# Kernel tuning notes

Measured on AMD Instinct MI355X. Metric: run time of the kernel, lower is better.

The kernel has to match this reference:

```python
import jax, jax.numpy as jnp
import numpy as np

B, S, D, H, MB = 2, 2048, 2048, 32, 16
HD = D // H          # 64
N = S // MB          # 128 mini-batches
EPS = 1e-5
BASE_LR = 1.0


def setup_inputs() -> dict:
    ks = jax.random.split(jax.random.key(0), 8)
    sc = 1.0 / np.sqrt(D)
    inv = 1.0 / (10000.0 ** (np.arange(0, HD, 2, dtype=np.float64) / HD))
    return {
        "x": jax.random.normal(ks[0], (B, S, D), jnp.float32),
        "pos_frequencies": jnp.asarray(np.outer(np.arange(S), inv), jnp.float32),  # (S, HD//2) rope angles
        "Wq": jax.random.normal(ks[1], (D, D), jnp.float32) * sc,
        "Wk": jax.random.normal(ks[2], (D, D), jnp.float32) * sc,
        "Wv": jax.random.normal(ks[3], (D, D), jnp.float32) * sc,
        "Wo": jax.random.normal(ks[4], (D, D), jnp.float32) * sc,
        "post_gamma": jnp.ones((D,), jnp.float32),
        "post_beta": jnp.zeros((D,), jnp.float32),
        "ilr_W": jax.random.normal(ks[5], (H, 1, D), jnp.float32) * 0.02,  # inner_loop_lr_W
        "ilr_b": jnp.zeros((H, 1), jnp.float32),                            # inner_loop_lr_b
        "lgs": jnp.zeros((MB,), jnp.float32),                               # learnable_gradient_scale
        "ttt_gamma": jnp.ones((H, HD), jnp.float32),                        # ttt_norm_weight
        "ttt_beta": jnp.zeros((H, HD), jnp.float32),                        # ttt_norm_bias
        "W0": jax.random.normal(ks[6], (H, HD, HD), jnp.float32) / np.sqrt(HD),
        "b0": jnp.zeros((H, 1, HD), jnp.float32),
    }


def _rope(x, freqs):
    # x: (B,H,S,HD), freqs: (S,HD//2); rotate interleaved pairs
    cos = jnp.cos(freqs)[None, None]
    sin = jnp.sin(freqs)[None, None]
    x1, x2 = x[..., 0::2], x[..., 1::2]
    return jnp.stack([x1 * cos - x2 * sin, x1 * sin + x2 * cos], -1).reshape(x.shape)


def _ln_fwd(z, g, b):
    mu = z.mean(-1, keepdims=True)
    var = z.var(-1, keepdims=True)
    return g * (z - mu) * jax.lax.rsqrt(var + EPS) + b


def _ln_l2_bwd(z, tgt, g, b):
    # grad of 0.5*||LN(z) - tgt||^2 w.r.t. z (fused LayerNorm backward)
    mu = z.mean(-1, keepdims=True)
    var = z.var(-1, keepdims=True)
    rstd = jax.lax.rsqrt(var + EPS)
    zh = (z - mu) * rstd
    dy = (g * zh + b) - tgt
    dzh = dy * g
    return (dzh - dzh.mean(-1, keepdims=True) - zh * (dzh * zh).mean(-1, keepdims=True)) * rstd


def reference(x, pos_frequencies, Wq, Wk, Wv, Wo, post_gamma, post_beta,
              ilr_W, ilr_b, lgs, ttt_gamma, ttt_beta, W0, b0):
    # projections (torch Linear: x @ W.T), shape (B,H,S,HD)
    q = (x @ Wq.T).reshape(B, S, H, HD).transpose(0, 2, 1, 3)
    k = (x @ Wk.T).reshape(B, S, H, HD).transpose(0, 2, 1, 3)
    v = (x @ Wv.T).reshape(B, S, H, HD).transpose(0, 2, 1, 3)
    q = _rope(q, pos_frequencies)
    k = _rope(k, pos_frequencies)
    v = _rope(v, pos_frequencies)  # module applies RoPE to V too

    # inner-loop learning rates: (B,H,N,1,MB), gradient_scale: (MB,1)
    xr = x.reshape(B, N, MB, D)
    lr = jnp.einsum('bnkd,hod->bhnko', xr, ilr_W) + ilr_b.reshape(1, H, 1, 1, 1)
    lr = BASE_LR * jax.nn.sigmoid(lr).transpose(0, 1, 2, 4, 3) / HD
    gs = jnp.clip(1.0 / jnp.arange(1, MB + 1, dtype=jnp.float32) + lgs, 0.0)
    eta = gs.reshape(1, 1, 1, MB, 1) * lr  # (B,H,N,MB,MB)

    to_n = lambda t: t.reshape(B, H, N, MB, -1).transpose(2, 0, 1, 3, 4)
    Qn, Kn, Vn = to_n(q), to_n(k), to_n(v)           # (N,B,H,MB,HD)
    En = eta.transpose(2, 0, 1, 3, 4)                # (N,B,H,MB,MB)

    g = ttt_gamma.reshape(1, H, 1, HD)
    be = ttt_beta.reshape(1, H, 1, HD)
    W_init = jnp.broadcast_to(W0[None], (B, H, HD, HD))
    b_init = jnp.broadcast_to(b0[None], (B, H, 1, HD))

    def step(carry, inp):
        W, bb = carry
        XQ, XK, XV, E = inp
        Z = XK @ W + bb
        grad = _ln_l2_bwd(Z, XV - XK, g, be)                 # (B,H,MB,HD)
        Attn = jnp.tril(XQ @ XK.swapaxes(-1, -2))            # causal dual form
        b_bar = bb - jnp.tril(E) @ grad
        Z_bar = XQ @ W - (E * Attn) @ grad + b_bar
        last_eta = E[..., -1, :, None]                       # (B,H,MB,1)
        W_new = W - jnp.swapaxes(last_eta * XK, -1, -2) @ grad
        b_new = bb - jnp.sum(last_eta * grad, axis=-2, keepdims=True)
        return (W_new, b_new), XQ + _ln_fwd(Z_bar, g, be)

    _, ys = jax.lax.scan(step, (W_init, b_init), (Qn, Kn, Vn, En))  # ys: (N,B,H,MB,HD)
    out = ys.transpose(1, 0, 3, 2, 4).reshape(B, S, D)

    mu = out.mean(-1, keepdims=True)
    var = out.var(-1, keepdims=True)
    out = post_gamma * (out - mu) * jax.lax.rsqrt(var + EPS) + post_beta
    return out @ Wo.T
```

## Files before the change

kernel.cpp:

```cpp
#include <hip/hip_runtime.h>
#include <hip/hip_bf16.h>
#include <math.h>

#define BB 2
#define SS 2048
#define DD 2048
#define HH 32
#define HDD 64
#define MBB 16
#define NN 128

typedef unsigned short u16;
typedef short bf16x8_t __attribute__((ext_vector_type(8)));
typedef float f32x4_t __attribute__((ext_vector_type(4)));

__device__ __forceinline__ float b2f(u16 u) { return __uint_as_float(((unsigned)u) << 16); }
__device__ __forceinline__ u16 f2b(float f) {
    unsigned u = __float_as_uint(f);
    return (u16)((u + 0x7FFFu + ((u >> 16) & 1u)) >> 16);
}
__device__ __forceinline__ unsigned pk2(float a, float b) {
    return (unsigned)f2b(a) | ((unsigned)f2b(b) << 16);
}
__device__ __forceinline__ unsigned cvtpk(float lo, float hi) {
    unsigned r;
    asm("v_cvt_pk_bf16_f32 %0, %1, %2" : "=v"(r) : "v"(lo), "v"(hi));
    return r;
}
__device__ __forceinline__ unsigned pk2r(u16 a, u16 b) { return (unsigned)a | ((unsigned)b << 16); }
__device__ __forceinline__ float wsum(float x) {
    x += __shfl_xor(x, 32);
    x += __shfl_xor(x, 16);
    x += __shfl_xor(x, 8);
    x += __shfl_xor(x, 4);
    x += __shfl_xor(x, 2);
    x += __shfl_xor(x, 1);
    return x;
}

template <int CTRL>
__device__ __forceinline__ float dppadd(float x) {
    int t = __builtin_amdgcn_update_dpp(0, __float_as_int(x), CTRL, 0xF, 0xF, true);
    return x + __int_as_float(t);
}
__device__ __forceinline__ float rsum16(float x) {
    x = dppadd<0xB1>(x);
    x = dppadd<0x4E>(x);
    x = dppadd<0x141>(x);
    x = dppadd<0x140>(x);
    return x;
}

typedef __attribute__((address_space(3))) unsigned int lds_u32;
typedef __attribute__((address_space(1))) const unsigned int glb_u32;
__device__ __forceinline__ void async_copy16(const void* g, void* l) {
    __builtin_amdgcn_global_load_lds((glb_u32*)g, (lds_u32*)l, 16, 0, 0);
}


__global__ __launch_bounds__(256) void k_cvt5(const float* __restrict__ x, const float* __restrict__ wq,
                                              const float* __restrict__ wk, const float* __restrict__ wv,
                                              const float* __restrict__ wo, u16* __restrict__ xb,
                                              u16* __restrict__ wqb, u16* __restrict__ wkb,
                                              u16* __restrict__ wvb, u16* __restrict__ wob) {
    int sl = blockIdx.y;
    long e = (long)(blockIdx.x * 256 + threadIdx.x) * 4;
    if (sl == 5) {
        long n = e >> 11;
        int cin = (int)(e & 2047);
        int hd0 = (cin >> 6) * 64 + ((cin & 63) >> 2);
        const float* src = wo + n * 2048 + hd0;
        float f0 = src[0], f1 = src[16], f2 = src[32], f3 = src[48];
        uint2 o;
        o.x = pk2(f0, f1);
        o.y = pk2(f2, f3);
        *(uint2*)(wob + e) = o;
        return;
    }
    const float* s;
    u16* d;
    if (sl == 0) { s = x; d = xb; }
    else if (sl == 1) { s = x + 4194304; d = xb + 4194304; }
    else if (sl == 2) { s = wq; d = wqb; }
    else if (sl == 3) { s = wk; d = wkb; }
    else { s = wv; d = wvb; }
    float4 f = *(const float4*)(s + e);
    uint2 o;
    o.x = pk2(f.x, f.y);
    o.y = pk2(f.z, f.w);
    *(uint2*)(d + e) = o;
}

__global__ void k_trig(const float* __restrict__ pf, float* __restrict__ ct, float* __restrict__ st) {
    int i = blockIdx.x * 256 + threadIdx.x;
    float f = pf[i];
    ct[i] = cosf(f);
    st[i] = sinf(f);
}

__global__ void k_ppg(const float* __restrict__ pg, const float* __restrict__ pb,
                      float* __restrict__ pgp, float* __restrict__ pbp) {
    int i = blockIdx.x * 256 + threadIdx.x;
    int h = i >> 6, o = i & 63;
    int src = h * 64 + (o >> 2) + (o & 3) * 16;
    pgp[i] = pg[src];
    pbp[i] = pb[src];
}

template <int EPI>
__global__ __launch_bounds__(256) void k_gemm_bt(const u16* __restrict__ A, const u16* __restrict__ B0,
                                                 const u16* __restrict__ B1, const u16* __restrict__ B2,
                                                 void* __restrict__ C0, void* __restrict__ C1,
                                                 void* __restrict__ C2, int M, int Nn, int K,
                                                 const float* __restrict__ ct, const float* __restrict__ st) {
    __shared__ u16 As[128 * 32];
    __shared__ u16 Bs[128 * 32];
    int z = blockIdx.z;
    const u16* Bm = (z == 0) ? B0 : (z == 1) ? B1 : B2;
    void* Cout = (z == 0) ? C0 : (z == 1) ? C1 : C2;
    int tid = threadIdx.x, lane = tid & 63, wv = tid >> 6;
    int m0 = blockIdx.y * 128, n0 = blockIdx.x * 128;
    int wm = wv >> 1, wn = wv & 1;

    f32x4_t acc[4][4];
    f32x4_t zero = {0.f, 0.f, 0.f, 0.f};
#pragma unroll
    for (int a = 0; a < 4; ++a)
#pragma unroll
        for (int b = 0; b < 4; ++b) acc[a][b] = zero;

    int mrow = lane & 15, qk = (lane >> 4) * 8;
    const int kTiles = K >> 5;
    for (int kt = 0; kt < kTiles; ++kt) {
        __syncthreads();
        int kb = kt << 5;
#pragma unroll
        for (int it = 0; it < 2; ++it) {
            int cb = it * 256 + wv * 64;
            int c = cb + lane;
            const u16* gpA = A + (m0 + (c >> 2)) * K + kb + ((c & 3) << 3);
            async_copy16(gpA, &As[cb << 3]);
            const u16* gpB = Bm + (n0 + (c >> 2)) * K + kb + ((c & 3) << 3);
            async_copy16(gpB, &Bs[cb << 3]);
        }
        asm volatile("s_waitcnt vmcnt(0)" ::: "memory");
        __syncthreads();

        bf16x8_t af[4], bfr[4];
#pragma unroll
        for (int mi = 0; mi < 4; ++mi)
            af[mi] = *(const bf16x8_t*)&As[(wm * 64 + mi * 16 + mrow) * 32 + qk];
#pragma unroll
        for (int ni = 0; ni < 4; ++ni)
            bfr[ni] = *(const bf16x8_t*)&Bs[(wn * 64 + ni * 16 + mrow) * 32 + qk];
#pragma unroll
        for (int mi = 0; mi < 4; ++mi)
#pragma unroll
            for (int ni = 0; ni < 4; ++ni)
                acc[mi][ni] = __builtin_amdgcn_mfma_f32_16x16x32_bf16(af[mi], bfr[ni], acc[mi][ni], 0, 0, 0);
    }

    int col16 = lane & 15, rq = (lane >> 4) * 4;
#pragma unroll
    for (int mi = 0; mi < 4; ++mi) {
#pragma unroll
        for (int ni = 0; ni < 4; ++ni) {
#pragma unroll
            for (int r = 0; r < 4; ++r) {
                int gr = m0 + wm * 64 + mi * 16 + rq + r;
                int gc = n0 + wn * 64 + ni * 16 + col16;
                float val = acc[mi][ni][r];
                if (EPI == 0) {
                    ((float*)Cout)[gr * Nn + gc] = val;
                } else {
                    int b = gr >> 11, s2 = gr & 2047, hh = gc >> 6, hd = gc & 63;
                    int fi = s2 * 32 + (hd >> 1);
                    float c = ct[fi], sn = st[fi];
                    float partner = __shfl_xor(val, 1);
                    float y = (gc & 1) ? (partner * sn + val * c) : (val * c - partner * sn);
                    int po = (z == 2) ? ((hd & 15) * 4 + (hd >> 4)) : hd;
                    ((u16*)Cout)[(((b * HH + hh) * SS) + s2) * HDD + po] = f2b(y);
                }
            }
        }
    }
}

__global__ __launch_bounds__(256) void k_lr(const u16* __restrict__ xb, const float* __restrict__ ilrW,
                                            const float* __restrict__ ilrb, float* __restrict__ lrout) {
    __shared__ u16 xr[4][2048];
    int row0 = blockIdx.x * 4;
    int tid = threadIdx.x, lane = tid & 63, wv = tid >> 6;
    const unsigned* src = (const unsigned*)(xb + row0 * 2048);
    unsigned* dst = (unsigned*)xr;
    for (int i = tid; i < 4096; i += 256) dst[i] = src[i];
    __syncthreads();
    int b = row0 >> 11, s0 = row0 & 2047;
#pragma unroll
    for (int sub = 0; sub < 8; ++sub) {
        int h = wv * 8 + sub;
        const float* wp = ilrW + h * 2048;
        float a0 = 0.f, a1 = 0.f, a2 = 0.f, a3 = 0.f;
        for (int i = 0; i < 16; ++i) {
            int idx = i * 128 + lane * 2;
            float2 w2 = *(const float2*)(wp + idx);
            unsigned p0 = *(const unsigned*)&xr[0][idx];
            unsigned p1 = *(const unsigned*)&xr[1][idx];
            unsigned p2 = *(const unsigned*)&xr[2][idx];
            unsigned p3 = *(const unsigned*)&xr[3][idx];
            a0 += b2f((u16)p0) * w2.x + b2f((u16)(p0 >> 16)) * w2.y;
            a1 += b2f((u16)p1) * w2.x + b2f((u16)(p1 >> 16)) * w2.y;
            a2 += b2f((u16)p2) * w2.x + b2f((u16)(p2 >> 16)) * w2.y;
            a3 += b2f((u16)p3) * w2.x + b2f((u16)(p3 >> 16)) * w2.y;
        }
        a0 = wsum(a0);
        a1 = wsum(a1);
        a2 = wsum(a2);
        a3 = wsum(a3);
        if (lane == 0) {
            float bv = ilrb[h];
            float* op = lrout + ((b * HH + h) * SS) + s0;
            op[0] = (1.0f / (1.0f + expf(-(a0 + bv)))) * (1.0f / 64.0f);
            op[1] = (1.0f / (1.0f + expf(-(a1 + bv)))) * (1.0f / 64.0f);
            op[2] = (1.0f / (1.0f + expf(-(a2 + bv)))) * (1.0f / 64.0f);
            op[3] = (1.0f / (1.0f + expf(-(a3 + bv)))) * (1.0f / 64.0f);
        }
    }
}

__global__ __launch_bounds__(64, 1) void k_scan(const u16* __restrict__ qb, const u16* __restrict__ kb2,
                                                const u16* __restrict__ vc, const float* __restrict__ lrbuf,
                                                const float* __restrict__ lgs, const float* __restrict__ tg,
                                                const float* __restrict__ tb, const float* __restrict__ W0,
                                                const float* __restrict__ b0, u16* __restrict__ ys) {
    __shared__ u16 WbL[64 * 72];
    __shared__ u16 XKT[64 * 40];
    __shared__ u16 GST[64 * 40];
    __shared__ u16 PUL[16 * 40];

    const int bh = blockIdx.x, h = bh & 31, b = bh >> 5;
    const int lane = threadIdx.x & 63;
    const int quad = lane >> 4, col = lane & 15;
    const int base = bh * SS;

    {
        unsigned* p1 = (unsigned*)XKT;
        unsigned* p2 = (unsigned*)GST;
        unsigned* p3 = (unsigned*)PUL;
        for (int i = lane; i < 1280; i += 64) { p1[i] = 0; p2[i] = 0; }
        for (int i = lane; i < 320; i += 64) p3[i] = 0;
    }

    float gd4[4], bd4[4], bbv[4], g2[4], gb[4];
#pragma unroll
    for (int tn = 0; tn < 4; ++tn) {
        gd4[tn] = tg[h * 64 + tn * 16 + col];
        bd4[tn] = tb[h * 64 + tn * 16 + col];
        bbv[tn] = b0[h * 64 + tn * 16 + col];
        g2[tn] = gd4[tn] * gd4[tn];
        gb[tn] = gd4[tn] * bd4[tn];
    }
    float G2m;
    {
        float s = g2[0] + g2[1] + g2[2] + g2[3];
        s = rsum16(s);
        G2m = s * (1.f / 64.f);
    }
    float gs4[4];
#pragma unroll
    for (int r = 0; r < 4; ++r) {
        int i = quad * 4 + r;
        gs4[r] = fmaxf(1.f / (float)(i + 1) + lgs[i], 0.f);
    }
    const float gs15 = fmaxf(1.f / 16.f + lgs[15], 0.f);

    f32x4_t Wc[4][4];
#pragma unroll
    for (int tm = 0; tm < 4; ++tm)
#pragma unroll
        for (int tn = 0; tn < 4; ++tn)
#pragma unroll
            for (int r = 0; r < 4; ++r)
                Wc[tm][tn][r] = W0[h * 4096 + (tm * 16 + quad * 4 + r) * 64 + tn * 16 + col];

    {
        unsigned* wb32 = (unsigned*)WbL;
#pragma unroll
        for (int tn = 0; tn < 4; ++tn)
#pragma unroll
            for (int tm = 0; tm < 4; ++tm) {
                int a = (tn * 16 + col) * 36 + tm * 8 + quad * 2;
                wb32[a] = cvtpk(Wc[tm][tn][0], Wc[tm][tn][1]);
                wb32[a + 1] = cvtpk(Wc[tm][tn][2], Wc[tm][tn][3]);
            }
    }

    bf16x8_t ka[2], qa[2];
    float lr4[4];
    u16 kraw[16], vraw[16], qraw[16];
    {
        const u16* kp = kb2 + (base + col) * 64;
        const u16* qp = qb + (base + col) * 64;
#pragma unroll
        for (int kh = 0; kh < 2; ++kh) {
            ka[kh] = *(const bf16x8_t*)(kp + kh * 32 + quad * 8);
            qa[kh] = *(const bf16x8_t*)(qp + kh * 32 + quad * 8);
        }
#pragma unroll
        for (int r = 0; r < 4; ++r) lr4[r] = lrbuf[base + quad * 4 + r];
#pragma unroll
        for (int tn = 0; tn < 4; ++tn)
#pragma unroll
            for (int r = 0; r < 4; ++r) {
                int idx = (base + quad * 4 + r) * 64 + tn * 16 + col;
                kraw[tn * 4 + r] = kb2[idx];
                qraw[tn * 4 + r] = qb[idx];
            }
#pragma unroll
        for (int r = 0; r < 4; ++r) {
            long ro = (long)(base + quad * 4 + r) * 64 + col * 4;
            ushort4 tv = *(const ushort4*)(vc + ro);
            vraw[r] = tv.x; vraw[4 + r] = tv.y; vraw[8 + r] = tv.z; vraw[12 + r] = tv.w;
        }
    }

    bf16x8_t xkf[4], wbf[4][2];
    {
        unsigned* x32 = (unsigned*)XKT;
#pragma unroll
        for (int tn = 0; tn < 4; ++tn) {
            int a = (tn * 16 + col) * 20 + quad * 2;
            x32[a] = pk2r(kraw[tn * 4 + 0], kraw[tn * 4 + 1]);
            x32[a + 1] = pk2r(kraw[tn * 4 + 2], kraw[tn * 4 + 3]);
        }
#pragma unroll
        for (int t = 0; t < 4; ++t)
            xkf[t] = *(const bf16x8_t*)&XKT[(t * 16 + col) * 40 + quad * 8];
#pragma unroll
        for (int tn = 0; tn < 4; ++tn)
#pragma unroll
            for (int kh = 0; kh < 2; ++kh)
                wbf[tn][kh] = *(const bf16x8_t*)&WbL[(tn * 16 + col) * 72 + kh * 32 + quad * 8];
    }

    const f32x4_t zf = {0.f, 0.f, 0.f, 0.f};

    for (int n = 0; n < NN; ++n) {
        const int s0 = n * 16;

        f32x4_t z[4], xqw[4], attn;
#pragma unroll
        for (int tn = 0; tn < 4; ++tn) {
            z[tn] = __builtin_amdgcn_mfma_f32_16x16x32_bf16(ka[1], wbf[tn][1], zf, 0, 0, 0);
            z[tn] = __builtin_amdgcn_mfma_f32_16x16x32_bf16(ka[0], wbf[tn][0], z[tn], 0, 0, 0);
            xqw[tn] = __builtin_amdgcn_mfma_f32_16x16x32_bf16(qa[1], wbf[tn][1], zf, 0, 0, 0);
            xqw[tn] = __builtin_amdgcn_mfma_f32_16x16x32_bf16(qa[0], wbf[tn][0], xqw[tn], 0, 0, 0);
        }
        attn = __builtin_amdgcn_mfma_f32_16x16x32_bf16(qa[1], ka[1], zf, 0, 0, 0);
        attn = __builtin_amdgcn_mfma_f32_16x16x32_bf16(qa[0], ka[0], attn, 0, 0, 0);

#pragma unroll
        for (int r = 0; r < 4; ++r) {
            float pv = (col <= quad * 4 + r) ? (1.f + attn[r]) : 0.f;
            PUL[(quad * 4 + r) * 40 + col] = f2b(pv);
        }

        bf16x8_t nka[2], nqa[2];
        float nlr[4];
        u16 nkraw[16], nvraw[16], nqraw[16];
        {
            const int sp = (n + 1 < NN) ? s0 + 16 : s0;
            const u16* kp = kb2 + (base + sp + col) * 64;
            const u16* qp = qb + (base + sp + col) * 64;
#pragma unroll
            for (int kh = 0; kh < 2; ++kh) {
                nka[kh] = *(const bf16x8_t*)(kp + kh * 32 + quad * 8);
                nqa[kh] = *(const bf16x8_t*)(qp + kh * 32 + quad * 8);
            }
#pragma unroll
            for (int r = 0; r < 4; ++r) nlr[r] = lrbuf[base + sp + quad * 4 + r];
#pragma unroll
            for (int tn = 0; tn < 4; ++tn)
#pragma unroll
                for (int r = 0; r < 4; ++r) {
                    int idx = (base + sp + quad * 4 + r) * 64 + tn * 16 + col;
                    nkraw[tn * 4 + r] = kb2[idx];
                    nqraw[tn * 4 + r] = qb[idx];
                }
#pragma unroll
            for (int r = 0; r < 4; ++r) {
                long ro = (long)(base + sp + quad * 4 + r) * 64 + col * 4;
                ushort4 tv = *(const ushort4*)(vc + ro);
                nvraw[r] = tv.x; nvraw[4 + r] = tv.y; nvraw[8 + r] = tv.z; nvraw[12 + r] = tv.w;
            }
        }

#pragma unroll
        for (int tn = 0; tn < 4; ++tn)
#pragma unroll
            for (int r = 0; r < 4; ++r) z[tn][r] += bbv[tn];

        float c1[16];
        float A1[4], A2[4], A3[4], A4[4], A5[4], A6[4];
#pragma unroll
        for (int r = 0; r < 4; ++r) { A1[r] = 0.f; A2[r] = 0.f; A3[r] = 0.f; A4[r] = 0.f; A5[r] = 0.f; A6[r] = 0.f; }
#pragma unroll
        for (int tn = 0; tn < 4; ++tn)
#pragma unroll
            for (int r = 0; r < 4; ++r) {
                float zv = z[tn][r];
                float tgt = b2f(vraw[tn * 4 + r]) - b2f(kraw[tn * 4 + r]);
                float c = gb[tn] - gd4[tn] * tgt;
                c1[tn * 4 + r] = c;
                float t = g2[tn] * zv;
                A1[r] += zv;
                A2[r] = fmaf(zv, zv, A2[r]);
                A3[r] += t;
                A4[r] = fmaf(t, zv, A4[r]);
                A5[r] = fmaf(c, zv, A5[r]);
                A6[r] += c;
            }
#pragma unroll
        for (int r = 0; r < 4; ++r) {
            A1[r] = rsum16(A1[r]);
            A2[r] = rsum16(A2[r]);
            A3[r] = rsum16(A3[r]);
            A4[r] = rsum16(A4[r]);
            A5[r] = rsum16(A5[r]);
            A6[r] = rsum16(A6[r]);
        }
        float mu4[4], rstd4[4], m1[4], m2[4], rl[4];
#pragma unroll
        for (int r = 0; r < 4; ++r) {
            float mu = A1[r] * (1.f / 64.f);
            float var = A2[r] * (1.f / 64.f) - mu * mu;
            float rstd = rsqrtf(var + 1e-5f);
            float T1m = A3[r] * (1.f / 64.f);
            float T2m = A4[r] * (1.f / 64.f);
            float T3m = A5[r] * (1.f / 64.f);
            float C1m = A6[r] * (1.f / 64.f);
            m1[r] = rstd * (T1m - mu * G2m) + C1m;
            m2[r] = rstd * rstd * (T2m - 2.f * mu * T1m + mu * mu * G2m) + rstd * (T3m - mu * C1m);
            mu4[r] = mu;
            rstd4[r] = rstd;
            rl[r] = rstd * lr4[r];
        }
        float gS[4][4];
#pragma unroll
        for (int tn = 0; tn < 4; ++tn)
#pragma unroll
            for (int r = 0; r < 4; ++r) {
                float zh = (z[tn][r] - mu4[r]) * rstd4[r];
                float dzh = fmaf(g2[tn], zh, c1[tn * 4 + r]);
                gS[tn][r] = fmaf(-m2[r], zh, dzh - m1[r]) * rl[r];
            }
        {
            unsigned* g32 = (unsigned*)GST;
#pragma unroll
            for (int tn = 0; tn < 4; ++tn) {
                int a = (tn * 16 + col) * 20 + quad * 2;
                g32[a] = cvtpk(gS[tn][0], gS[tn][1]);
                g32[a + 1] = cvtpk(gS[tn][2], gS[tn][3]);
            }
        }

        bf16x8_t gsf[4], puf;
#pragma unroll
        for (int t = 0; t < 4; ++t)
            gsf[t] = *(const bf16x8_t*)&GST[(t * 16 + col) * 40 + quad * 8];
        puf = *(const bf16x8_t*)&PUL[col * 40 + quad * 8];

#pragma unroll
        for (int tm = 0; tm < 4; ++tm)
#pragma unroll
            for (int tn = 0; tn < 4; ++tn) {
                f32x4_t dw = __builtin_amdgcn_mfma_f32_16x16x32_bf16(xkf[tm], gsf[tn], zf, 0, 0, 0);
#pragma unroll
                for (int r = 0; r < 4; ++r) Wc[tm][tn][r] -= gs15 * dw[r];
            }
        {
            unsigned* wb32 = (unsigned*)WbL;
#pragma unroll
            for (int tn = 0; tn < 4; ++tn)
#pragma unroll
                for (int tm = 0; tm < 4; ++tm) {
                    int a = (tn * 16 + col) * 36 + tm * 8 + quad * 2;
                    wb32[a] = cvtpk(Wc[tm][tn][0], Wc[tm][tn][1]);
                    wb32[a + 1] = cvtpk(Wc[tm][tn][2], Wc[tm][tn][3]);
                }
        }

#pragma unroll
        for (int tn = 0; tn < 4; ++tn) {
            f32x4_t pg = __builtin_amdgcn_mfma_f32_16x16x32_bf16(puf, gsf[tn], zf, 0, 0, 0);
#pragma unroll
            for (int r = 0; r < 4; ++r) z[tn][r] = xqw[tn][r] + bbv[tn] - gs4[r] * pg[r];
        }
#pragma unroll
        for (int r = 0; r < 4; ++r) {
            float s1 = z[0][r] + z[1][r] + z[2][r] + z[3][r];
            float s2 = z[0][r] * z[0][r] + z[1][r] * z[1][r] + z[2][r] * z[2][r] + z[3][r] * z[3][r];
            s1 = rsum16(s1);
            s2 = rsum16(s2);
            float mu = s1 * (1.f / 64.f);
            float var = s2 * (1.f / 64.f) - mu * mu;
            mu4[r] = mu;
            rstd4[r] = rsqrtf(var + 1e-5f);
        }
#pragma unroll
        for (int r = 0; r < 4; ++r) {
            float y0 = b2f(qraw[0 * 4 + r]) + gd4[0] * (z[0][r] - mu4[r]) * rstd4[r] + bd4[0];
            float y1 = b2f(qraw[1 * 4 + r]) + gd4[1] * (z[1][r] - mu4[r]) * rstd4[r] + bd4[1];
            float y2 = b2f(qraw[2 * 4 + r]) + gd4[2] * (z[2][r] - mu4[r]) * rstd4[r] + bd4[2];
            float y3 = b2f(qraw[3 * 4 + r]) + gd4[3] * (z[3][r] - mu4[r]) * rstd4[r] + bd4[3];
            uint2 po;
            po.x = cvtpk(y0, y1);
            po.y = cvtpk(y2, y3);
            *(uint2*)(ys + (long)(b * SS + s0 + quad * 4 + r) * DD + h * 64 + col * 4) = po;
        }

#pragma unroll
        for (int tn = 0; tn < 4; ++tn) {
            float c = gS[tn][0] + gS[tn][1] + gS[tn][2] + gS[tn][3];
            c += __shfl_xor(c, 16);
            c += __shfl_xor(c, 32);
            bbv[tn] -= gs15 * c;
        }

        {
            unsigned* x32 = (unsigned*)XKT;
#pragma unroll
            for (int tn = 0; tn < 4; ++tn) {
                int a = (tn * 16 + col) * 20 + quad * 2;
                x32[a] = pk2r(nkraw[tn * 4 + 0], nkraw[tn * 4 + 1]);
                x32[a + 1] = pk2r(nkraw[tn * 4 + 2], nkraw[tn * 4 + 3]);
            }
#pragma unroll
            for (int t = 0; t < 4; ++t)
                xkf[t] = *(const bf16x8_t*)&XKT[(t * 16 + col) * 40 + quad * 8];
#pragma unroll
            for (int tn = 0; tn < 4; ++tn)
#pragma unroll
                for (int kh = 0; kh < 2; ++kh)
                    wbf[tn][kh] = *(const bf16x8_t*)&WbL[(tn * 16 + col) * 72 + kh * 32 + quad * 8];
        }

        ka[0] = nka[0]; ka[1] = nka[1];
        qa[0] = nqa[0]; qa[1] = nqa[1];
#pragma unroll
        for (int r = 0; r < 4; ++r) lr4[r] = nlr[r];
#pragma unroll
        for (int j = 0; j < 16; ++j) { kraw[j] = nkraw[j]; vraw[j] = nvraw[j]; qraw[j] = nqraw[j]; }
    }
}

__global__ __launch_bounds__(256) void k_postln(const u16* __restrict__ ys, const float* __restrict__ pg,
                                                const float* __restrict__ pb, u16* __restrict__ outb) {
    __shared__ float red[8];
    int row = blockIdx.x, tid = threadIdx.x, lane = tid & 63, wv = tid >> 6;
    const u16* rp = ys + row * 2048 + tid * 8;
    uint4 pkd = *(const uint4*)rp;
    float v[8];
    v[0] = b2f((u16)pkd.x); v[1] = b2f((u16)(pkd.x >> 16));
    v[2] = b2f((u16)pkd.y); v[3] = b2f((u16)(pkd.y >> 16));
    v[4] = b2f((u16)pkd.z); v[5] = b2f((u16)(pkd.z >> 16));
    v[6] = b2f((u16)pkd.w); v[7] = b2f((u16)(pkd.w >> 16));
    float s1 = 0.f, s2 = 0.f;
#pragma unroll
    for (int i = 0; i < 8; ++i) { s1 += v[i]; s2 += v[i] * v[i]; }
    s1 = wsum(s1);
    s2 = wsum(s2);
    if (lane == 0) {
        red[wv] = s1;
        red[wv + 4] = s2;
    }
    __syncthreads();
    float S1 = red[0] + red[1] + red[2] + red[3];
    float S2 = red[4] + red[5] + red[6] + red[7];
    float mu = S1 * (1.f / 2048), var = S2 * (1.f / 2048) - mu * mu;
    float rstd = rsqrtf(var + 1e-5f);
    const float4 g0 = *(const float4*)(pg + tid * 8);
    const float4 g1 = *(const float4*)(pg + tid * 8 + 4);
    const float4 b0v = *(const float4*)(pb + tid * 8);
    const float4 b1v = *(const float4*)(pb + tid * 8 + 4);
    float o[8];
    o[0] = g0.x * (v[0] - mu) * rstd + b0v.x;
    o[1] = g0.y * (v[1] - mu) * rstd + b0v.y;
    o[2] = g0.z * (v[2] - mu) * rstd + b0v.z;
    o[3] = g0.w * (v[3] - mu) * rstd + b0v.w;
    o[4] = g1.x * (v[4] - mu) * rstd + b1v.x;
    o[5] = g1.y * (v[5] - mu) * rstd + b1v.y;
    o[6] = g1.z * (v[6] - mu) * rstd + b1v.z;
    o[7] = g1.w * (v[7] - mu) * rstd + b1v.w;
    uint4 po;
    po.x = pk2(o[0], o[1]);
    po.y = pk2(o[2], o[3]);
    po.z = pk2(o[4], o[5]);
    po.w = pk2(o[6], o[7]);
    *(uint4*)(outb + row * 2048 + tid * 8) = po;
}

extern "C" void kernel_launch(void* const* d_in, const int* in_sizes, int n_in,
                              void* d_out, int out_size, void* d_ws, size_t ws_size,
                              hipStream_t stream) {
    const float* x = (const float*)d_in[0];
    const float* pf = (const float*)d_in[1];
    const float* Wq = (const float*)d_in[2];
    const float* Wk = (const float*)d_in[3];
    const float* Wv = (const float*)d_in[4];
    const float* Wo = (const float*)d_in[5];
    const float* pg = (const float*)d_in[6];
    const float* pb = (const float*)d_in[7];
    const float* ilrW = (const float*)d_in[8];
    const float* ilrb = (const float*)d_in[9];
    const float* lgs = (const float*)d_in[10];
    const float* tg = (const float*)d_in[11];
    const float* tb = (const float*)d_in[12];
    const float* W0 = (const float*)d_in[13];
    const float* b0 = (const float*)d_in[14];
    float* out = (float*)d_out;
    char* ws = (char*)d_ws;

    u16* xbf = (u16*)(ws + 0);
    u16* wqb = (u16*)(ws + 16777216);
    u16* wkb = (u16*)(ws + 25165824);
    u16* wvb = (u16*)(ws + 33554432);
    u16* wob = (u16*)(ws + 41943040);
    u16* qbuf = (u16*)(ws + 50331648);
    u16* kbuf = (u16*)(ws + 67108864);
    u16* vbuf = (u16*)(ws + 83886080);
    float* ct = (float*)(ws + 100663296);
    float* st = (float*)(ws + 100925440);
    float* lrb = (float*)(ws + 101187584);
    u16* ysb = (u16*)(ws + 101711872);
    float* pgp = (float*)(ws + 118489088);
    float* pbp = (float*)(ws + 118497280);
    u16* lnb = (u16*)(ws + 0);

    k_cvt5<<<dim3(4096, 6), 256, 0, stream>>>(x, Wq, Wk, Wv, Wo, xbf, wqb, wkb, wvb, wob);
    k_trig<<<256, 256, 0, stream>>>(pf, ct, st);
    k_ppg<<<8, 256, 0, stream>>>(pg, pb, pgp, pbp);

    k_gemm_bt<1><<<dim3(16, 32, 3), 256, 0, stream>>>(xbf, wqb, wkb, wvb, qbuf, kbuf, vbuf,
                                                      4096, 2048, 2048, ct, st);

    k_lr<<<1024, 256, 0, stream>>>(xbf, ilrW, ilrb, lrb);

    k_scan<<<64, 64, 0, stream>>>(qbuf, kbuf, vbuf, lrb, lgs, tg, tb, W0, b0, ysb);

    k_postln<<<4096, 256, 0, stream>>>(ysb, pgp, pbp, lnb);
    k_gemm_bt<0><<<dim3(16, 32, 1), 256, 0, stream>>>(lnb, wob, wob, wob, out, out, out,
                                                      4096, 2048, 2048, nullptr, nullptr);
}
```

Baseline: 740.6 us.

## Feed scan MFMAs from registers with 16x16x16 bf16, drop LDS staging

```diff
diff --git a/kernel.cpp b/kernel.cpp
--- a/kernel.cpp
+++ b/kernel.cpp
@@ -12,6 +12,7 @@
 
 typedef unsigned short u16;
 typedef short bf16x8_t __attribute__((ext_vector_type(8)));
+typedef short bf16x4_t __attribute__((ext_vector_type(4)));
 typedef float f32x4_t __attribute__((ext_vector_type(4)));
 
 __device__ __forceinline__ float b2f(u16 u) { return __uint_as_float(((unsigned)u) << 16); }
@@ -28,6 +29,14 @@
     return r;
 }
 __device__ __forceinline__ unsigned pk2r(u16 a, u16 b) { return (unsigned)a | ((unsigned)b << 16); }
+__device__ __forceinline__ bf16x4_t mk4(unsigned lo, unsigned hi) {
+    union { unsigned u[2]; bf16x4_t v; } t;
+    t.u[0] = lo;
+    t.u[1] = hi;
+    return t.v;
+}
+#define MFMA16(A, B, C) __builtin_amdgcn_mfma_f32_16x16x16bf16_1k((A), (B), (C), 0, 0, 0)
+
 __device__ __forceinline__ float wsum(float x) {
     x += __shfl_xor(x, 32);
     x += __shfl_xor(x, 16);
@@ -234,22 +243,11 @@
                                                 const float* __restrict__ tb, const float* __restrict__ W0,
                                                 const float* __restrict__ b0, u16* __restrict__ ys) {
     __shared__ u16 WbL[64 * 72];
-    __shared__ u16 XKT[64 * 40];
-    __shared__ u16 GST[64 * 40];
-    __shared__ u16 PUL[16 * 40];
 
     const int bh = blockIdx.x, h = bh & 31, b = bh >> 5;
     const int lane = threadIdx.x & 63;
     const int quad = lane >> 4, col = lane & 15;
     const int base = bh * SS;
-
-    {
-        unsigned* p1 = (unsigned*)XKT;
-        unsigned* p2 = (unsigned*)GST;
-        unsigned* p3 = (unsigned*)PUL;
-        for (int i = lane; i < 1280; i += 64) { p1[i] = 0; p2[i] = 0; }
-        for (int i = lane; i < 320; i += 64) p3[i] = 0;
-    }
 
     float gd4[4], bd4[4], bbv[4], g2[4], gb[4];
 #pragma unroll
@@ -266,13 +264,15 @@
         s = rsum16(s);
         G2m = s * (1.f / 64.f);
     }
-    float gs4[4];
+    const float gs15 = fmaxf(1.f / 16.f + lgs[15], 0.f);
+    const float inv15 = gs15 > 0.f ? 1.f / gs15 : 0.f;
+    float gs4[4], ratio4[4];
 #pragma unroll
     for (int r = 0; r < 4; ++r) {
         int i = quad * 4 + r;
         gs4[r] = fmaxf(1.f / (float)(i + 1) + lgs[i], 0.f);
-    }
-    const float gs15 = fmaxf(1.f / 16.f + lgs[15], 0.f);
+        ratio4[r] = gs4[r] * inv15;
+    }
 
     f32x4_t Wc[4][4];
 #pragma unroll
@@ -307,7 +307,7 @@
             qa[kh] = *(const bf16x8_t*)(qp + kh * 32 + quad * 8);
         }
 #pragma unroll
-        for (int r = 0; r < 4; ++r) lr4[r] = lrbuf[base + quad * 4 + r];
+        for (int r = 0; r < 4; ++r) lr4[r] = -gs15 * lrbuf[base + quad * 4 + r];
 #pragma unroll
         for (int tn = 0; tn < 4; ++tn)
 #pragma unroll
@@ -324,46 +324,35 @@
         }
     }
 
-    bf16x8_t xkf[4], wbf[4][2];
-    {
-        unsigned* x32 = (unsigned*)XKT;
-#pragma unroll
-        for (int tn = 0; tn < 4; ++tn) {
-            int a = (tn * 16 + col) * 20 + quad * 2;
-            x32[a] = pk2r(kraw[tn * 4 + 0], kraw[tn * 4 + 1]);
-            x32[a + 1] = pk2r(kraw[tn * 4 + 2], kraw[tn * 4 + 3]);
-        }
-#pragma unroll
-        for (int t = 0; t < 4; ++t)
-            xkf[t] = *(const bf16x8_t*)&XKT[(t * 16 + col) * 40 + quad * 8];
-#pragma unroll
-        for (int tn = 0; tn < 4; ++tn)
-#pragma unroll
-            for (int kh = 0; kh < 2; ++kh)
-                wbf[tn][kh] = *(const bf16x8_t*)&WbL[(tn * 16 + col) * 72 + kh * 32 + quad * 8];
-    }
+    bf16x8_t wbf[4][2];
+#pragma unroll
+    for (int tn = 0; tn < 4; ++tn)
+#pragma unroll
+        for (int kh = 0; kh < 2; ++kh)
+            wbf[tn][kh] = *(const bf16x8_t*)&WbL[(tn * 16 + col) * 72 + kh * 32 + quad * 8];
 
     const f32x4_t zf = {0.f, 0.f, 0.f, 0.f};
 
     for (int n = 0; n < NN; ++n) {
         const int s0 = n * 16;
 
-        f32x4_t z[4], xqw[4], attn;
+        f32x4_t z[4], xqw[4], attnT;
 #pragma unroll
         for (int tn = 0; tn < 4; ++tn) {
-            z[tn] = __builtin_amdgcn_mfma_f32_16x16x32_bf16(ka[1], wbf[tn][1], zf, 0, 0, 0);
+            f32x4_t cb = {bbv[tn], bbv[tn], bbv[tn], bbv[tn]};
+            z[tn] = __builtin_amdgcn_mfma_f32_16x16x32_bf16(ka[1], wbf[tn][1], cb, 0, 0, 0);
             z[tn] = __builtin_amdgcn_mfma_f32_16x16x32_bf16(ka[0], wbf[tn][0], z[tn], 0, 0, 0);
-            xqw[tn] = __builtin_amdgcn_mfma_f32_16x16x32_bf16(qa[1], wbf[tn][1], zf, 0, 0, 0);
+            xqw[tn] = __builtin_amdgcn_mfma_f32_16x16x32_bf16(qa[1], wbf[tn][1], cb, 0, 0, 0);
             xqw[tn] = __builtin_amdgcn_mfma_f32_16x16x32_bf16(qa[0], wbf[tn][0], xqw[tn], 0, 0, 0);
         }
-        attn = __builtin_amdgcn_mfma_f32_16x16x32_bf16(qa[1], ka[1], zf, 0, 0, 0);
-        attn = __builtin_amdgcn_mfma_f32_16x16x32_bf16(qa[0], ka[0], attn, 0, 0, 0);
-
-#pragma unroll
-        for (int r = 0; r < 4; ++r) {
-            float pv = (col <= quad * 4 + r) ? (1.f + attn[r]) : 0.f;
-            PUL[(quad * 4 + r) * 40 + col] = f2b(pv);
-        }
+        attnT = __builtin_amdgcn_mfma_f32_16x16x32_bf16(ka[1], qa[1], zf, 0, 0, 0);
+        attnT = __builtin_amdgcn_mfma_f32_16x16x32_bf16(ka[0], qa[0], attnT, 0, 0, 0);
+
+        float pv0 = (quad * 4 + 0 <= col) ? (1.f + attnT[0]) : 0.f;
+        float pv1 = (quad * 4 + 1 <= col) ? (1.f + attnT[1]) : 0.f;
+        float pv2 = (quad * 4 + 2 <= col) ? (1.f + attnT[2]) : 0.f;
+        float pv3 = (quad * 4 + 3 <= col) ? (1.f + attnT[3]) : 0.f;
+        bf16x4_t pa4 = mk4(cvtpk(pv0, pv1), cvtpk(pv2, pv3));
 
         bf16x8_t nka[2], nqa[2];
         float nlr[4];
@@ -378,7 +367,7 @@
                 nqa[kh] = *(const bf16x8_t*)(qp + kh * 32 + quad * 8);
             }
 #pragma unroll
-            for (int r = 0; r < 4; ++r) nlr[r] = lrbuf[base + sp + quad * 4 + r];
+            for (int r = 0; r < 4; ++r) nlr[r] = -gs15 * lrbuf[base + sp + quad * 4 + r];
 #pragma unroll
             for (int tn = 0; tn < 4; ++tn)
 #pragma unroll
@@ -394,11 +383,6 @@
                 nvraw[r] = tv.x; nvraw[4 + r] = tv.y; nvraw[8 + r] = tv.z; nvraw[12 + r] = tv.w;
             }
         }
-
-#pragma unroll
-        for (int tn = 0; tn < 4; ++tn)
-#pragma unroll
-            for (int r = 0; r < 4; ++r) z[tn][r] += bbv[tn];
 
         float c1[16];
         float A1[4], A2[4], A3[4], A4[4], A5[4], A6[4];
@@ -454,30 +438,18 @@
                 float dzh = fmaf(g2[tn], zh, c1[tn * 4 + r]);
                 gS[tn][r] = fmaf(-m2[r], zh, dzh - m1[r]) * rl[r];
             }
-        {
-            unsigned* g32 = (unsigned*)GST;
-#pragma unroll
-            for (int tn = 0; tn < 4; ++tn) {
-                int a = (tn * 16 + col) * 20 + quad * 2;
-                g32[a] = cvtpk(gS[tn][0], gS[tn][1]);
-                g32[a + 1] = cvtpk(gS[tn][2], gS[tn][3]);
-            }
-        }
-
-        bf16x8_t gsf[4], puf;
-#pragma unroll
-        for (int t = 0; t < 4; ++t)
-            gsf[t] = *(const bf16x8_t*)&GST[(t * 16 + col) * 40 + quad * 8];
-        puf = *(const bf16x8_t*)&PUL[col * 40 + quad * 8];
+        bf16x4_t gsB[4], xk4[4];
+#pragma unroll
+        for (int tn = 0; tn < 4; ++tn) {
+            gsB[tn] = mk4(cvtpk(gS[tn][0], gS[tn][1]), cvtpk(gS[tn][2], gS[tn][3]));
+            xk4[tn] = mk4(pk2r(kraw[tn * 4 + 0], kraw[tn * 4 + 1]), pk2r(kraw[tn * 4 + 2], kraw[tn * 4 + 3]));
+        }
 
 #pragma unroll
         for (int tm = 0; tm < 4; ++tm)
 #pragma unroll
-            for (int tn = 0; tn < 4; ++tn) {
-                f32x4_t dw = __builtin_amdgcn_mfma_f32_16x16x32_bf16(xkf[tm], gsf[tn], zf, 0, 0, 0);
-#pragma unroll
-                for (int r = 0; r < 4; ++r) Wc[tm][tn][r] -= gs15 * dw[r];
-            }
+            for (int tn = 0; tn < 4; ++tn)
+                Wc[tm][tn] = MFMA16(xk4[tm], gsB[tn], Wc[tm][tn]);
         {
             unsigned* wb32 = (unsigned*)WbL;
 #pragma unroll
@@ -492,9 +464,9 @@
 
 #pragma unroll
         for (int tn = 0; tn < 4; ++tn) {
-            f32x4_t pg = __builtin_amdgcn_mfma_f32_16x16x32_bf16(puf, gsf[tn], zf, 0, 0, 0);
-#pragma unroll
-            for (int r = 0; r < 4; ++r) z[tn][r] = xqw[tn][r] + bbv[tn] - gs4[r] * pg[r];
+            f32x4_t pg = MFMA16(pa4, gsB[tn], zf);
+#pragma unroll
+            for (int r = 0; r < 4; ++r) z[tn][r] = fmaf(ratio4[r], pg[r], xqw[tn][r]);
         }
 #pragma unroll
         for (int r = 0; r < 4; ++r) {
@@ -524,26 +496,14 @@
             float c = gS[tn][0] + gS[tn][1] + gS[tn][2] + gS[tn][3];
             c += __shfl_xor(c, 16);
             c += __shfl_xor(c, 32);
-            bbv[tn] -= gs15 * c;
-        }
-
-        {
-            unsigned* x32 = (unsigned*)XKT;
-#pragma unroll
-            for (int tn = 0; tn < 4; ++tn) {
-                int a = (tn * 16 + col) * 20 + quad * 2;
-                x32[a] = pk2r(nkraw[tn * 4 + 0], nkraw[tn * 4 + 1]);
-                x32[a + 1] = pk2r(nkraw[tn * 4 + 2], nkraw[tn * 4 + 3]);
-            }
-#pragma unroll
-            for (int t = 0; t < 4; ++t)
-                xkf[t] = *(const bf16x8_t*)&XKT[(t * 16 + col) * 40 + quad * 8];
-#pragma unroll
-            for (int tn = 0; tn < 4; ++tn)
-#pragma unroll
-                for (int kh = 0; kh < 2; ++kh)
-                    wbf[tn][kh] = *(const bf16x8_t*)&WbL[(tn * 16 + col) * 72 + kh * 32 + quad * 8];
-        }
+            bbv[tn] += c;
+        }
+
+#pragma unroll
+        for (int tn = 0; tn < 4; ++tn)
+#pragma unroll
+            for (int kh = 0; kh < 2; ++kh)
+                wbf[tn][kh] = *(const bf16x8_t*)&WbL[(tn * 16 + col) * 72 + kh * 32 + quad * 8];
 
         ka[0] = nka[0]; ka[1] = nka[1];
         qa[0] = nqa[0]; qa[1] = nqa[1];
```

Result: no change. 742.1 us (+0.2%).
